# Kernel tuning notes

Measured on AMD Instinct MI355X. Metric: run time of the kernel, lower is better.

Reference implementation:

```python
import jax, jax.numpy as jnp
import numpy as np


def _mlp2(x, W1, b1, W2, b2):
    # ReluMLP with two Dense layers: relu between layers, linear output
    return jax.nn.relu(x @ W1 + b1) @ W2 + b2


def setup_inputs() -> dict:
    key = jax.random.key(0)
    N, NP, DIN, D = 100000, 25000, 16, 64
    E, EDS, EP, EUS = 1_600_000, 800_000, 400_000, 200_000
    L = 8  # number of message-passing layers actually used
    ks = iter(jax.random.split(key, 40))
    nrm = lambda shape: jax.random.normal(next(ks), shape, jnp.float32) * 0.05
    ri = lambda n, hi: jax.random.randint(next(ks), (n,), 0, hi)
    return dict(
        x=jax.random.normal(next(ks), (N, DIN), jnp.float32),
        We1=nrm((DIN, D)), be1=jnp.zeros((D,), jnp.float32),
        We2=nrm((D, D)), be2=jnp.zeros((D,), jnp.float32),
        Wm1=nrm((L, D, D)), bm1=jnp.zeros((L, D), jnp.float32),
        Wm2=nrm((L, D, D)), bm2=jnp.zeros((L, D), jnp.float32),
        Wn1=nrm((L, 2 * D, D)), bn1=jnp.zeros((L, D), jnp.float32),
        Wn2=nrm((L, D, D)), bn2=jnp.zeros((L, D), jnp.float32),
        Wd1=nrm((D, D)), bd1=jnp.zeros((D,), jnp.float32),
        Wd2=nrm((D, 2)), bd2=jnp.zeros((2,), jnp.float32),
        s_fine=ri(E, N), r_fine=ri(E, N),
        s_ds=ri(EDS, N), r_ds=ri(EDS, N),
        s_p=ri(EP, NP), r_p=ri(EP, NP),
        s_us=ri(EUS, NP), r_us=ri(EUS, NP),
        uppool=ri(N, NP), downpool=ri(NP, NP),
    )


def reference(x, We1, be1, We2, be2, Wm1, bm1, Wm2, bm2, Wn1, bn1, Wn2, bn2,
              Wd1, bd1, Wd2, bd2, s_fine, r_fine, s_ds, r_ds, s_p, r_p,
              s_us, r_us, uppool, downpool):
    def mp(l, h, s, r, n):
        # LinearMessagePassingLayer: message MLP on sender feats,
        # sum-scatter to receivers (mean_aggr=False), node MLP on [h, aggr]
        msg = _mlp2(h[s], Wm1[l], bm1[l], Wm2[l], bm2[l])          # [E, D]
        aggr = jax.ops.segment_sum(msg, r, num_segments=n)          # [n, D]
        return _mlp2(jnp.concatenate([h, aggr], -1),
                     Wn1[l], bn1[l], Wn2[l], bn2[l])                # [n, D]

    N = x.shape[0]
    NP = downpool.shape[0]
    # encode
    h = _mlp2(x, We1, be1, We2, be2)                                 # [N, D]
    h = mp(0, h, s_fine, r_fine, N)
    h = mp(1, h, s_fine, r_fine, N)
    skip = h
    # Downsample: gather by uppool idx, MP on downsampling graph, select pooled
    g = mp(2, h[uppool], s_ds, r_ds, N)                              # [N, D]
    hp = g[downpool]                                                 # [NP, D]
    # bottleneck
    hp = mp(3, hp, s_p, r_p, NP)
    hp = mp(4, hp, s_p, r_p, NP)
    # Upsample: gather by downpool idx, MP on upsampling graph, select by uppool
    g = mp(5, hp[downpool], s_us, r_us, NP)                          # [NP, D]
    h = g[uppool]                                                    # [N, D]
    # decode with skip connections
    h = mp(6, h, s_fine, r_fine, N) + skip
    h = mp(7, h, s_fine, r_fine, N) + skip
    return _mlp2(h, Wd1, bd1, Wd2, bd2)                              # [N, 2]
```

## Files before the change

### kernel.cpp

```cpp
#include <hip/hip_runtime.h>

#define WG 256

#define MLP_FMA16(ACC, A, W) do { \
    ACC[0][0]=fmaf(A.x,W.x,ACC[0][0]); ACC[0][1]=fmaf(A.x,W.y,ACC[0][1]); \
    ACC[0][2]=fmaf(A.x,W.z,ACC[0][2]); ACC[0][3]=fmaf(A.x,W.w,ACC[0][3]); \
    ACC[1][0]=fmaf(A.y,W.x,ACC[1][0]); ACC[1][1]=fmaf(A.y,W.y,ACC[1][1]); \
    ACC[1][2]=fmaf(A.y,W.z,ACC[1][2]); ACC[1][3]=fmaf(A.y,W.w,ACC[1][3]); \
    ACC[2][0]=fmaf(A.z,W.x,ACC[2][0]); ACC[2][1]=fmaf(A.z,W.y,ACC[2][1]); \
    ACC[2][2]=fmaf(A.z,W.z,ACC[2][2]); ACC[2][3]=fmaf(A.z,W.w,ACC[2][3]); \
    ACC[3][0]=fmaf(A.w,W.x,ACC[3][0]); ACC[3][1]=fmaf(A.w,W.y,ACC[3][1]); \
    ACC[3][2]=fmaf(A.w,W.z,ACC[3][2]); ACC[3][3]=fmaf(A.w,W.w,ACC[3][3]); \
} while (0)

template<int DINA, bool HAS_B, bool HAS_SKIP, bool GATHER_A,
         int MSG_DOUT, bool PARTIAL_MSG, bool WRITE_OUT1>
__global__ __launch_bounds__(WG)
void mlp2_fused(const float* __restrict__ inA, const int* __restrict__ gidxA,
                const float* __restrict__ inB,
                const float* __restrict__ W1, const float* __restrict__ b1,
                const float* __restrict__ W2, const float* __restrict__ b2,
                const float* __restrict__ skip, float* __restrict__ out1,
                const float* __restrict__ M1, const float* __restrict__ mb1,
                const float* __restrict__ M2, const float* __restrict__ mb2,
                float* __restrict__ outM, int msgN, int n)
{
    constexpr int XP = 68;
    __shared__ __align__(16) float sXT[64][XP];
    __shared__ __align__(16) float sW[64 * 64];
    __shared__ float sb[128];
    __shared__ float sW2d[128];
    __shared__ float sb2d[2];

    const int tid = threadIdx.x;
    const int tx = tid & 15, ty = tid >> 4;
    const int c0 = tx * 4, r0 = ty * 4;
    const int row0 = blockIdx.x * 64;
    const int lrow = tid & 63;
    const int kq0 = (tid >> 6) * 4;

    for (int i = tid * 4; i < DINA * 64; i += WG * 4)
        *(float4*)&sW[i] = *(const float4*)&W1[i];
    if (tid < 64) sb[tid] = b1[tid];
    else if (tid < 128) sb[tid] = b2[tid - 64];

    {
        const int rg = min(row0 + lrow, n - 1);
        const int ra = GATHER_A ? gidxA[rg] : rg;
        const float* pA = inA + (size_t)ra * DINA;
        #pragma unroll
        for (int kq = kq0; kq < DINA; kq += 16) {
            const float4 v = *(const float4*)(pA + kq);
            sXT[kq + 0][lrow] = v.x; sXT[kq + 1][lrow] = v.y;
            sXT[kq + 2][lrow] = v.z; sXT[kq + 3][lrow] = v.w;
        }
    }
    __syncthreads();

    float acc[4][4] = {};
    #pragma unroll 8
    for (int k = 0; k < DINA; ++k) {
        const float4 a = *(const float4*)&sXT[k][r0];
        const float4 w = *(const float4*)&sW[k * 64 + c0];
        MLP_FMA16(acc, a, w);
    }

    if constexpr (HAS_B) {
        __syncthreads();
        for (int i = tid * 4; i < 64 * 64; i += WG * 4)
            *(float4*)&sW[i] = *(const float4*)&W1[DINA * 64 + i];
        {
            const int rg = min(row0 + lrow, n - 1);
            const float* pB = inB + (size_t)rg * 64;
            #pragma unroll
            for (int kq = kq0; kq < 64; kq += 16) {
                const float4 v = *(const float4*)(pB + kq);
                sXT[kq + 0][lrow] = v.x; sXT[kq + 1][lrow] = v.y;
                sXT[kq + 2][lrow] = v.z; sXT[kq + 3][lrow] = v.w;
            }
        }
        __syncthreads();
        #pragma unroll 8
        for (int k = 0; k < 64; ++k) {
            const float4 a = *(const float4*)&sXT[k][r0];
            const float4 w = *(const float4*)&sW[k * 64 + c0];
            MLP_FMA16(acc, a, w);
        }
    }
    __syncthreads();

    for (int i = tid * 4; i < 64 * 64; i += WG * 4)
        *(float4*)&sW[i] = *(const float4*)&W2[i];
    #pragma unroll
    for (int j = 0; j < 4; ++j) {
        const float bj = sb[c0 + j];
        *(float4*)&sXT[c0 + j][r0] = make_float4(
            fmaxf(acc[0][j] + bj, 0.f), fmaxf(acc[1][j] + bj, 0.f),
            fmaxf(acc[2][j] + bj, 0.f), fmaxf(acc[3][j] + bj, 0.f));
    }
    __syncthreads();

    float acc2[4][4] = {};
    #pragma unroll 8
    for (int k = 0; k < 64; ++k) {
        const float4 a = *(const float4*)&sXT[k][r0];
        const float4 w = *(const float4*)&sW[k * 64 + c0];
        MLP_FMA16(acc2, a, w);
    }

    float ofull[4][4];
    #pragma unroll
    for (int i = 0; i < 4; ++i) {
        const int row = row0 + r0 + i;
        float4 s = make_float4(0.f, 0.f, 0.f, 0.f);
        if (HAS_SKIP && row < n) s = *(const float4*)&skip[(size_t)row * 64 + c0];
        ofull[i][0] = acc2[i][0] + sb[64 + c0 + 0] + s.x;
        ofull[i][1] = acc2[i][1] + sb[64 + c0 + 1] + s.y;
        ofull[i][2] = acc2[i][2] + sb[64 + c0 + 2] + s.z;
        ofull[i][3] = acc2[i][3] + sb[64 + c0 + 3] + s.w;
        if (WRITE_OUT1 && row < n)
            *(float4*)&out1[(size_t)row * 64 + c0] =
                make_float4(ofull[i][0], ofull[i][1], ofull[i][2], ofull[i][3]);
    }

    if constexpr (MSG_DOUT > 0) {
        if (!PARTIAL_MSG || row0 < msgN) {
            __syncthreads();
            for (int i = tid * 4; i < 64 * 64; i += WG * 4)
                *(float4*)&sW[i] = *(const float4*)&M1[i];
            if (tid < 64) sb[tid] = mb1[tid];
            if constexpr (MSG_DOUT == 64) {
                if (tid >= 64 && tid < 128) sb[tid] = mb2[tid - 64];
            } else {
                if (tid >= 64 && tid < 192) sW2d[tid - 64] = M2[tid - 64];
                if (tid >= 192 && tid < 194) sb2d[tid - 192] = mb2[tid - 192];
            }
            #pragma unroll
            for (int j = 0; j < 4; ++j)
                *(float4*)&sXT[c0 + j][r0] =
                    make_float4(ofull[0][j], ofull[1][j], ofull[2][j], ofull[3][j]);
            __syncthreads();

            float acc3[4][4] = {};
            #pragma unroll 8
            for (int k = 0; k < 64; ++k) {
                const float4 a = *(const float4*)&sXT[k][r0];
                const float4 w = *(const float4*)&sW[k * 64 + c0];
                MLP_FMA16(acc3, a, w);
            }
            __syncthreads();
            if constexpr (MSG_DOUT == 64) {
                for (int i = tid * 4; i < 64 * 64; i += WG * 4)
                    *(float4*)&sW[i] = *(const float4*)&M2[i];
            }
            #pragma unroll
            for (int j = 0; j < 4; ++j) {
                const float bj = sb[c0 + j];
                *(float4*)&sXT[c0 + j][r0] = make_float4(
                    fmaxf(acc3[0][j] + bj, 0.f), fmaxf(acc3[1][j] + bj, 0.f),
                    fmaxf(acc3[2][j] + bj, 0.f), fmaxf(acc3[3][j] + bj, 0.f));
            }
            __syncthreads();

            if constexpr (MSG_DOUT == 64) {
                float accM[4][4] = {};
                #pragma unroll 8
                for (int k = 0; k < 64; ++k) {
                    const float4 a = *(const float4*)&sXT[k][r0];
                    const float4 w = *(const float4*)&sW[k * 64 + c0];
                    MLP_FMA16(accM, a, w);
                }
                #pragma unroll
                for (int i = 0; i < 4; ++i) {
                    const int row = row0 + r0 + i;
                    if (row < msgN)
                        *(float4*)&outM[(size_t)row * 64 + c0] =
                            make_float4(accM[i][0] + sb[64 + c0 + 0],
                                        accM[i][1] + sb[64 + c0 + 1],
                                        accM[i][2] + sb[64 + c0 + 2],
                                        accM[i][3] + sb[64 + c0 + 3]);
                }
            } else {
                if (tid < 128) {
                    const int lr = tid >> 1, col = tid & 1;
                    float o0 = sb2d[col], o1 = 0.0f;
                    #pragma unroll 8
                    for (int k = 0; k < 64; k += 2) {
                        o0 = fmaf(sXT[k][lr],     sW2d[k * 2 + col],       o0);
                        o1 = fmaf(sXT[k + 1][lr], sW2d[(k + 1) * 2 + col], o1);
                    }
                    const int row = row0 + lr;
                    if (row < msgN) outM[(size_t)row * 2 + col] = o0 + o1;
                }
            }
        }
    }
}

template<int DINA, bool HAS_B, bool HAS_SKIP, bool GATHER_A>
__global__ __launch_bounds__(WG)
void mlp2_rt(const float* __restrict__ inA, const int* __restrict__ gidxA,
             const float* __restrict__ inB,
             const float* __restrict__ W1, const float* __restrict__ b1,
             const float* __restrict__ W2, const float* __restrict__ b2,
             const float* __restrict__ skip,
             float* __restrict__ out, int n)
{
    constexpr int XP = 68;
    __shared__ __align__(16) float sXT[64][XP];
    __shared__ __align__(16) float sW[64 * 64];
    __shared__ float sb[128];

    const int tid = threadIdx.x;
    const int tx = tid & 15, ty = tid >> 4;
    const int c0 = tx * 4, r0 = ty * 4;
    const int row0 = blockIdx.x * 64;
    const int lrow = tid & 63;
    const int kq0 = (tid >> 6) * 4;

    for (int i = tid * 4; i < DINA * 64; i += WG * 4)
        *(float4*)&sW[i] = *(const float4*)&W1[i];
    if (tid < 64) sb[tid] = b1[tid];
    else if (tid < 128) sb[tid] = b2[tid - 64];

    {
        const int rg = min(row0 + lrow, n - 1);
        const int ra = GATHER_A ? gidxA[rg] : rg;
        const float* pA = inA + (size_t)ra * DINA;
        #pragma unroll
        for (int kq = kq0; kq < DINA; kq += 16) {
            const float4 v = *(const float4*)(pA + kq);
            sXT[kq + 0][lrow] = v.x; sXT[kq + 1][lrow] = v.y;
            sXT[kq + 2][lrow] = v.z; sXT[kq + 3][lrow] = v.w;
        }
    }
    __syncthreads();

    float acc[4][4] = {};
    #pragma unroll 8
    for (int k = 0; k < DINA; ++k) {
        const float4 a = *(const float4*)&sXT[k][r0];
        const float4 w = *(const float4*)&sW[k * 64 + c0];
        MLP_FMA16(acc, a, w);
    }
    if constexpr (HAS_B) {
        __syncthreads();
        for (int i = tid * 4; i < 64 * 64; i += WG * 4)
            *(float4*)&sW[i] = *(const float4*)&W1[DINA * 64 + i];
        {
            const int rg = min(row0 + lrow, n - 1);
            const float* pB = inB + (size_t)rg * 64;
            #pragma unroll
            for (int kq = kq0; kq < 64; kq += 16) {
                const float4 v = *(const float4*)(pB + kq);
                sXT[kq + 0][lrow] = v.x; sXT[kq + 1][lrow] = v.y;
                sXT[kq + 2][lrow] = v.z; sXT[kq + 3][lrow] = v.w;
            }
        }
        __syncthreads();
        #pragma unroll 8
        for (int k = 0; k < 64; ++k) {
            const float4 a = *(const float4*)&sXT[k][r0];
            const float4 w = *(const float4*)&sW[k * 64 + c0];
            MLP_FMA16(acc, a, w);
        }
    }
    __syncthreads();

    for (int i = tid * 4; i < 64 * 64; i += WG * 4)
        *(float4*)&sW[i] = *(const float4*)&W2[i];
    #pragma unroll
    for (int j = 0; j < 4; ++j) {
        const float bj = sb[c0 + j];
        *(float4*)&sXT[c0 + j][r0] = make_float4(
            fmaxf(acc[0][j] + bj, 0.f), fmaxf(acc[1][j] + bj, 0.f),
            fmaxf(acc[2][j] + bj, 0.f), fmaxf(acc[3][j] + bj, 0.f));
    }
    __syncthreads();

    float acc2[4][4] = {};
    #pragma unroll 8
    for (int k = 0; k < 64; ++k) {
        const float4 a = *(const float4*)&sXT[k][r0];
        const float4 w = *(const float4*)&sW[k * 64 + c0];
        MLP_FMA16(acc2, a, w);
    }
    #pragma unroll
    for (int i = 0; i < 4; ++i) {
        const int row = row0 + r0 + i;
        if (row < n) {
            float4 o = make_float4(acc2[i][0] + sb[64 + c0 + 0],
                                   acc2[i][1] + sb[64 + c0 + 1],
                                   acc2[i][2] + sb[64 + c0 + 2],
                                   acc2[i][3] + sb[64 + c0 + 3]);
            if (HAS_SKIP) {
                const float4 s = *(const float4*)&skip[(size_t)row * 64 + c0];
                o.x += s.x; o.y += s.y; o.z += s.z; o.w += s.w;
            }
            *(float4*)&out[(size_t)row * 64 + c0] = o;
        }
    }
}

__global__ __launch_bounds__(WG)
void slot_fill_xcd_k(const int* __restrict__ s, const int* __restrict__ r,
                     int* __restrict__ cursor, int* __restrict__ slots,
                     int cap, int E, int n)
{
    const int xcd = blockIdx.x & 7;
    const int w   = blockIdx.x >> 3;
    const int W   = gridDim.x >> 3;
    const int lo  = (int)(((long)n * xcd) >> 3);
    const int hi  = (int)(((long)n * (xcd + 1)) >> 3);
    const int chunk = (E + W - 1) / W;
    const int e0 = w * chunk;
    const int e1 = min(E, e0 + chunk);
    for (int e = e0 + (int)threadIdx.x; e < e1; e += WG) {
        const int v = __builtin_nontemporal_load(&r[e]);
        if (v >= lo && v < hi) {
            const int sv = __builtin_nontemporal_load(&s[e]);
            const int p = atomicAdd(&cursor[v], 1);
            if (p < cap) slots[(size_t)v * cap + p] = sv;
        }
    }
}

template<bool REMAP>
__global__ __launch_bounds__(WG)
void gather_slots_k(const int* __restrict__ deg, const int* __restrict__ slots,
                    int cap, const int* __restrict__ remap,
                    const float* __restrict__ tab, float* __restrict__ aggr, int n)
{
    const int node = blockIdx.x * (WG / 64) + (threadIdx.x >> 6);
    const int c = threadIdx.x & 63;
    if (node >= n) return;
    const int d = min(deg[node], cap);
    const int* sl = slots + (size_t)node * cap;

    int myidx = 0;
    if (c < d) {
        myidx = __builtin_nontemporal_load(&sl[c]);
        if (REMAP) myidx = remap[myidx];
    }

    float a[8] = {};
    int j = 0;
    for (; j + 7 < d; j += 8) {
        #pragma unroll
        for (int u = 0; u < 8; ++u) {
            const int t = __shfl(myidx, j + u);
            a[u] += tab[(size_t)t * 64 + c];
        }
    }
    #pragma unroll 4
    for (; j < d; ++j) {
        const int t = __shfl(myidx, j);
        a[j & 7] += tab[(size_t)t * 64 + c];
    }
    aggr[(size_t)node * 64 + c] =
        ((a[0] + a[1]) + (a[2] + a[3])) + ((a[4] + a[5]) + (a[6] + a[7]));
}

extern "C" void kernel_launch(void* const* d_in, const int* in_sizes, int n_in,
                              void* d_out, int out_size, void* d_ws, size_t ws_size,
                              hipStream_t stream)
{
    const float* x    = (const float*)d_in[0];
    const float* We1  = (const float*)d_in[1];
    const float* be1  = (const float*)d_in[2];
    const float* We2  = (const float*)d_in[3];
    const float* be2  = (const float*)d_in[4];
    const float* Wm1  = (const float*)d_in[5];
    const float* bm1  = (const float*)d_in[6];
    const float* Wm2  = (const float*)d_in[7];
    const float* bm2  = (const float*)d_in[8];
    const float* Wn1  = (const float*)d_in[9];
    const float* bn1  = (const float*)d_in[10];
    const float* Wn2  = (const float*)d_in[11];
    const float* bn2  = (const float*)d_in[12];
    const float* Wd1  = (const float*)d_in[13];
    const float* bd1  = (const float*)d_in[14];
    const float* Wd2  = (const float*)d_in[15];
    const float* bd2  = (const float*)d_in[16];
    const int* s_fine = (const int*)d_in[17];
    const int* r_fine = (const int*)d_in[18];
    const int* s_ds   = (const int*)d_in[19];
    const int* r_ds   = (const int*)d_in[20];
    const int* s_p    = (const int*)d_in[21];
    const int* r_p    = (const int*)d_in[22];
    const int* s_us   = (const int*)d_in[23];
    const int* r_us   = (const int*)d_in[24];
    const int* uppool   = (const int*)d_in[25];
    const int* downpool = (const int*)d_in[26];

    const int N   = in_sizes[0] / 16;
    const int E   = in_sizes[17];
    const int EDS = in_sizes[19];
    const int EP  = in_sizes[21];
    const int EUS = in_sizes[23];
    const int NP  = in_sizes[26];

    const int CAP_FINE = 48, CAP_DS = 32, CAP_PP = 48, CAP_US = 32;

    float* B0  = (float*)d_ws;
    float* B1  = B0 + (size_t)N * 64;
    float* B2  = B1 + (size_t)N * 64;
    float* B3  = B2 + (size_t)N * 64;
    float* HPa = B3 + (size_t)N * 64;
    float* HPb = HPa + (size_t)NP * 64;
    int* ip = (int*)(HPb + (size_t)NP * 64);
    auto alloc_i = [&](size_t n) { int* p = ip; ip += n; return p; };
    int* cur_fine = alloc_i(N);
    int* cur_ds   = alloc_i(N);
    int* cur_pp   = alloc_i(NP);
    int* cur_us   = alloc_i(NP);
    int* sl_fine  = alloc_i((size_t)N * CAP_FINE);
    int* sl_ds    = alloc_i((size_t)N * CAP_DS);
    int* sl_pp    = alloc_i((size_t)NP * CAP_PP);
    int* sl_us    = alloc_i((size_t)NP * CAP_US);

    const int gN  = (N + 63) / 64;
    const int gNP = (NP + 63) / 64;
    const int gaN  = (N + 3) / 4;
    const int gaNP = (NP + 3) / 4;

    hipMemsetAsync(cur_fine, 0, (size_t)(2 * N + 2 * NP) * sizeof(int), stream);
    slot_fill_xcd_k<<<2048, WG, 0, stream>>>(s_fine, r_fine, cur_fine, sl_fine, CAP_FINE, E,   N);
    slot_fill_xcd_k<<<1024, WG, 0, stream>>>(s_ds,   r_ds,   cur_ds,   sl_ds,   CAP_DS,   EDS, N);
    slot_fill_xcd_k<<<512,  WG, 0, stream>>>(s_p,    r_p,    cur_pp,   sl_pp,   CAP_PP,   EP,  NP);
    slot_fill_xcd_k<<<512,  WG, 0, stream>>>(s_us,   r_us,   cur_us,   sl_us,   CAP_US,   EUS, NP);

    mlp2_fused<16,false,false,false,64,false,true><<<gN,WG,0,stream>>>(
        x,nullptr,nullptr, We1,be1,We2,be2, nullptr,B0,
        Wm1+0*4096,bm1+0*64,Wm2+0*4096,bm2+0*64, B1, N, N);
    gather_slots_k<false><<<gaN,WG,0,stream>>>(cur_fine,sl_fine,CAP_FINE,nullptr,B1,B2,N);

    mlp2_fused<64,true,false,false,64,false,true><<<gN,WG,0,stream>>>(
        B0,nullptr,B2, Wn1+0*8192,bn1+0*64,Wn2+0*4096,bn2+0*64, nullptr,B3,
        Wm1+1*4096,bm1+1*64,Wm2+1*4096,bm2+1*64, B0, N, N);
    gather_slots_k<false><<<gaN,WG,0,stream>>>(cur_fine,sl_fine,CAP_FINE,nullptr,B0,B2,N);

    mlp2_fused<64,true,false,false,64,true,true><<<gN,WG,0,stream>>>(
        B3,nullptr,B2, Wn1+1*8192,bn1+1*64,Wn2+1*4096,bn2+1*64, nullptr,B1,
        Wm1+2*4096,bm1+2*64,Wm2+2*4096,bm2+2*64, B0, NP, N);
    gather_slots_k<true><<<gaN,WG,0,stream>>>(cur_ds,sl_ds,CAP_DS,uppool,B0,B2,N);

    mlp2_rt<64,true,false,true><<<gN,WG,0,stream>>>(
        B1,uppool,B2, Wn1+2*8192,bn1+2*64,Wn2+2*4096,bn2+2*64, nullptr,B3,N);

    mlp2_rt<64,false,false,true><<<gNP,WG,0,stream>>>(
        B3,downpool,nullptr, Wm1+3*4096,bm1+3*64,Wm2+3*4096,bm2+3*64, nullptr,HPa,NP);
    gather_slots_k<false><<<gaNP,WG,0,stream>>>(cur_pp,sl_pp,CAP_PP,nullptr,HPa,B2,NP);

    mlp2_fused<64,true,false,true,64,false,true><<<gNP,WG,0,stream>>>(
        B3,downpool,B2, Wn1+3*8192,bn1+3*64,Wn2+3*4096,bn2+3*64, nullptr,HPb,
        Wm1+4*4096,bm1+4*64,Wm2+4*4096,bm2+4*64, HPa, NP, NP);
    gather_slots_k<false><<<gaNP,WG,0,stream>>>(cur_pp,sl_pp,CAP_PP,nullptr,HPa,B2,NP);

    mlp2_fused<64,true,false,false,64,false,true><<<gNP,WG,0,stream>>>(
        HPb,nullptr,B2, Wn1+4*8192,bn1+4*64,Wn2+4*4096,bn2+4*64, nullptr,HPa,
        Wm1+5*4096,bm1+5*64,Wm2+5*4096,bm2+5*64, HPb, NP, NP);
    gather_slots_k<true><<<gaNP,WG,0,stream>>>(cur_us,sl_us,CAP_US,downpool,HPb,B2,NP);

    mlp2_fused<64,true,false,true,64,false,true><<<gNP,WG,0,stream>>>(
        HPa,downpool,B2, Wn1+5*8192,bn1+5*64,Wn2+5*4096,bn2+5*64, nullptr,HPb,
        Wm1+6*4096,bm1+6*64,Wm2+6*4096,bm2+6*64, B3, NP, NP);
    gather_slots_k<true><<<gaN,WG,0,stream>>>(cur_fine,sl_fine,CAP_FINE,uppool,B3,B2,N);

    mlp2_fused<64,true,true,true,64,false,true><<<gN,WG,0,stream>>>(
        HPb,uppool,B2, Wn1+6*8192,bn1+6*64,Wn2+6*4096,bn2+6*64, B1,B0,
        Wm1+7*4096,bm1+7*64,Wm2+7*4096,bm2+7*64, B3, N, N);
    gather_slots_k<false><<<gaN,WG,0,stream>>>(cur_fine,sl_fine,CAP_FINE,nullptr,B3,B2,N);

    mlp2_fused<64,true,true,false,2,false,false><<<gN,WG,0,stream>>>(
        B0,nullptr,B2, Wn1+7*8192,bn1+7*64,Wn2+7*4096,bn2+7*64, B1,nullptr,
        Wd1,bd1,Wd2,bd2, (float*)d_out, N, N);
}
```

Before: 1.064 ms.

## Fuse slot-based neighbor aggregation into node-MLP kernels, drop separate gather kernels

```diff
diff --git a/kernel.cpp b/kernel.cpp
--- a/kernel.cpp
+++ b/kernel.cpp
@@ -13,11 +13,13 @@
     ACC[3][2]=fmaf(A.w,W.z,ACC[3][2]); ACC[3][3]=fmaf(A.w,W.w,ACC[3][3]); \
 } while (0)
 
-template<int DINA, bool HAS_B, bool HAS_SKIP, bool GATHER_A,
+template<int DINA, bool HAS_AGGR, bool REMAPB, bool HAS_SKIP, bool GATHER_A,
          int MSG_DOUT, bool PARTIAL_MSG, bool WRITE_OUT1>
 __global__ __launch_bounds__(WG)
 void mlp2_fused(const float* __restrict__ inA, const int* __restrict__ gidxA,
-                const float* __restrict__ inB,
+                const int* __restrict__ deg, const int* __restrict__ slots,
+                int cap, const int* __restrict__ remapB,
+                const float* __restrict__ tab,
                 const float* __restrict__ W1, const float* __restrict__ b1,
                 const float* __restrict__ W2, const float* __restrict__ b2,
                 const float* __restrict__ skip, float* __restrict__ out1,
@@ -36,8 +38,9 @@
     const int tx = tid & 15, ty = tid >> 4;
     const int c0 = tx * 4, r0 = ty * 4;
     const int row0 = blockIdx.x * 64;
-    const int lrow = tid & 63;
-    const int kq0 = (tid >> 6) * 4;
+    const int lane = tid & 63;
+    const int wv = tid >> 6;
+    const int kq0 = wv * 4;
 
     for (int i = tid * 4; i < DINA * 64; i += WG * 4)
         *(float4*)&sW[i] = *(const float4*)&W1[i];
@@ -45,14 +48,46 @@
     else if (tid < 128) sb[tid] = b2[tid - 64];
 
     {
-        const int rg = min(row0 + lrow, n - 1);
+        const int rg = min(row0 + lane, n - 1);
         const int ra = GATHER_A ? gidxA[rg] : rg;
         const float* pA = inA + (size_t)ra * DINA;
         #pragma unroll
         for (int kq = kq0; kq < DINA; kq += 16) {
             const float4 v = *(const float4*)(pA + kq);
-            sXT[kq + 0][lrow] = v.x; sXT[kq + 1][lrow] = v.y;
-            sXT[kq + 2][lrow] = v.z; sXT[kq + 3][lrow] = v.w;
+            sXT[kq + 0][lane] = v.x; sXT[kq + 1][lane] = v.y;
+            sXT[kq + 2][lane] = v.z; sXT[kq + 3][lane] = v.w;
+        }
+    }
+
+    float av[16];
+    if constexpr (HAS_AGGR) {
+        #pragma unroll
+        for (int i = 0; i < 16; ++i) {
+            const int node = min(row0 + wv * 16 + i, n - 1);
+            const int d = min(deg[node], cap);
+            const int* sl = slots + (size_t)node * cap;
+            int myidx = 0;
+            if (lane < d) {
+                myidx = sl[lane];
+                if (REMAPB) myidx = remapB[myidx];
+            }
+            float a0 = 0.f, a1 = 0.f, a2 = 0.f, a3 = 0.f;
+            int j = 0;
+            for (; j + 3 < d; j += 4) {
+                const int t0 = __shfl(myidx, j + 0);
+                const int t1 = __shfl(myidx, j + 1);
+                const int t2 = __shfl(myidx, j + 2);
+                const int t3 = __shfl(myidx, j + 3);
+                a0 += tab[(size_t)t0 * 64 + lane];
+                a1 += tab[(size_t)t1 * 64 + lane];
+                a2 += tab[(size_t)t2 * 64 + lane];
+                a3 += tab[(size_t)t3 * 64 + lane];
+            }
+            for (; j < d; ++j) {
+                const int t = __shfl(myidx, j);
+                a0 += tab[(size_t)t * 64 + lane];
+            }
+            av[i] = (a0 + a1) + (a2 + a3);
         }
     }
     __syncthreads();
@@ -65,20 +100,13 @@
         MLP_FMA16(acc, a, w);
     }
 
-    if constexpr (HAS_B) {
+    if constexpr (HAS_AGGR) {
         __syncthreads();
         for (int i = tid * 4; i < 64 * 64; i += WG * 4)
             *(float4*)&sW[i] = *(const float4*)&W1[DINA * 64 + i];
-        {
-            const int rg = min(row0 + lrow, n - 1);
-            const float* pB = inB + (size_t)rg * 64;
-            #pragma unroll
-            for (int kq = kq0; kq < 64; kq += 16) {
-                const float4 v = *(const float4*)(pB + kq);
-                sXT[kq + 0][lrow] = v.x; sXT[kq + 1][lrow] = v.y;
-                sXT[kq + 2][lrow] = v.z; sXT[kq + 3][lrow] = v.w;
-            }
-        }
+        #pragma unroll
+        for (int i = 0; i < 16; ++i)
+            sXT[lane][wv * 16 + i] = av[i];
         __syncthreads();
         #pragma unroll 8
         for (int k = 0; k < 64; ++k) {
@@ -128,12 +156,13 @@
             __syncthreads();
             for (int i = tid * 4; i < 64 * 64; i += WG * 4)
                 *(float4*)&sW[i] = *(const float4*)&M1[i];
-            if (tid < 64) sb[tid] = mb1[tid];
             if constexpr (MSG_DOUT == 64) {
-                if (tid >= 64 && tid < 128) sb[tid] = mb2[tid - 64];
+                if (tid < 64) sb[tid] = mb1[tid];
+                else if (tid < 128) sb[tid] = mb2[tid - 64];
             } else {
-                if (tid >= 64 && tid < 192) sW2d[tid - 64] = M2[tid - 64];
-                if (tid >= 192 && tid < 194) sb2d[tid - 192] = mb2[tid - 192];
+                if (tid < 64) sb[tid] = mb1[tid];
+                else if (tid < 192) sW2d[tid - 64] = M2[tid - 64];
+                else if (tid < 194) sb2d[tid - 192] = mb2[tid - 192];
             }
             #pragma unroll
             for (int j = 0; j < 4; ++j)
@@ -197,111 +226,6 @@
     }
 }
 
-template<int DINA, bool HAS_B, bool HAS_SKIP, bool GATHER_A>
-__global__ __launch_bounds__(WG)
-void mlp2_rt(const float* __restrict__ inA, const int* __restrict__ gidxA,
-             const float* __restrict__ inB,
-             const float* __restrict__ W1, const float* __restrict__ b1,
-             const float* __restrict__ W2, const float* __restrict__ b2,
-             const float* __restrict__ skip,
-             float* __restrict__ out, int n)
-{
-    constexpr int XP = 68;
-    __shared__ __align__(16) float sXT[64][XP];
-    __shared__ __align__(16) float sW[64 * 64];
-    __shared__ float sb[128];
-
-    const int tid = threadIdx.x;
-    const int tx = tid & 15, ty = tid >> 4;
-    const int c0 = tx * 4, r0 = ty * 4;
-    const int row0 = blockIdx.x * 64;
-    const int lrow = tid & 63;
-    const int kq0 = (tid >> 6) * 4;
-
-    for (int i = tid * 4; i < DINA * 64; i += WG * 4)
-        *(float4*)&sW[i] = *(const float4*)&W1[i];
-    if (tid < 64) sb[tid] = b1[tid];
-    else if (tid < 128) sb[tid] = b2[tid - 64];
-
-    {
-        const int rg = min(row0 + lrow, n - 1);
-        const int ra = GATHER_A ? gidxA[rg] : rg;
-        const float* pA = inA + (size_t)ra * DINA;
-        #pragma unroll
-        for (int kq = kq0; kq < DINA; kq += 16) {
-            const float4 v = *(const float4*)(pA + kq);
-            sXT[kq + 0][lrow] = v.x; sXT[kq + 1][lrow] = v.y;
-            sXT[kq + 2][lrow] = v.z; sXT[kq + 3][lrow] = v.w;
-        }
-    }
-    __syncthreads();
-
-    float acc[4][4] = {};
-    #pragma unroll 8
-    for (int k = 0; k < DINA; ++k) {
-        const float4 a = *(const float4*)&sXT[k][r0];
-        const float4 w = *(const float4*)&sW[k * 64 + c0];
-        MLP_FMA16(acc, a, w);
-    }
-    if constexpr (HAS_B) {
-        __syncthreads();
-        for (int i = tid * 4; i < 64 * 64; i += WG * 4)
-            *(float4*)&sW[i] = *(const float4*)&W1[DINA * 64 + i];
-        {
-            const int rg = min(row0 + lrow, n - 1);
-            const float* pB = inB + (size_t)rg * 64;
-            #pragma unroll
-            for (int kq = kq0; kq < 64; kq += 16) {
-                const float4 v = *(const float4*)(pB + kq);
-                sXT[kq + 0][lrow] = v.x; sXT[kq + 1][lrow] = v.y;
-                sXT[kq + 2][lrow] = v.z; sXT[kq + 3][lrow] = v.w;
-            }
-        }
-        __syncthreads();
-        #pragma unroll 8
-        for (int k = 0; k < 64; ++k) {
-            const float4 a = *(const float4*)&sXT[k][r0];
-            const float4 w = *(const float4*)&sW[k * 64 + c0];
-            MLP_FMA16(acc, a, w);
-        }
-    }
-    __syncthreads();
-
-    for (int i = tid * 4; i < 64 * 64; i += WG * 4)
-        *(float4*)&sW[i] = *(const float4*)&W2[i];
-    #pragma unroll
-    for (int j = 0; j < 4; ++j) {
-        const float bj = sb[c0 + j];
-        *(float4*)&sXT[c0 + j][r0] = make_float4(
-            fmaxf(acc[0][j] + bj, 0.f), fmaxf(acc[1][j] + bj, 0.f),
-            fmaxf(acc[2][j] + bj, 0.f), fmaxf(acc[3][j] + bj, 0.f));
-    }
-    __syncthreads();
-
-    float acc2[4][4] = {};
-    #pragma unroll 8
-    for (int k = 0; k < 64; ++k) {
-        const float4 a = *(const float4*)&sXT[k][r0];
-        const float4 w = *(const float4*)&sW[k * 64 + c0];
-        MLP_FMA16(acc2, a, w);
-    }
-    #pragma unroll
-    for (int i = 0; i < 4; ++i) {
-        const int row = row0 + r0 + i;
-        if (row < n) {
-            float4 o = make_float4(acc2[i][0] + sb[64 + c0 + 0],
-                                   acc2[i][1] + sb[64 + c0 + 1],
-                                   acc2[i][2] + sb[64 + c0 + 2],
-                                   acc2[i][3] + sb[64 + c0 + 3]);
-            if (HAS_SKIP) {
-                const float4 s = *(const float4*)&skip[(size_t)row * 64 + c0];
-                o.x += s.x; o.y += s.y; o.z += s.z; o.w += s.w;
-            }
-            *(float4*)&out[(size_t)row * 64 + c0] = o;
-        }
-    }
-}
-
 __global__ __launch_bounds__(WG)
 void slot_fill_xcd_k(const int* __restrict__ s, const int* __restrict__ r,
                      int* __restrict__ cursor, int* __restrict__ slots,
@@ -323,42 +247,6 @@
             if (p < cap) slots[(size_t)v * cap + p] = sv;
         }
     }
-}
-
-template<bool REMAP>
-__global__ __launch_bounds__(WG)
-void gather_slots_k(const int* __restrict__ deg, const int* __restrict__ slots,
-                    int cap, const int* __restrict__ remap,
-                    const float* __restrict__ tab, float* __restrict__ aggr, int n)
-{
-    const int node = blockIdx.x * (WG / 64) + (threadIdx.x >> 6);
-    const int c = threadIdx.x & 63;
-    if (node >= n) return;
-    const int d = min(deg[node], cap);
-    const int* sl = slots + (size_t)node * cap;
-
-    int myidx = 0;
-    if (c < d) {
-        myidx = __builtin_nontemporal_load(&sl[c]);
-        if (REMAP) myidx = remap[myidx];
-    }
-
-    float a[8] = {};
-    int j = 0;
-    for (; j + 7 < d; j += 8) {
-        #pragma unroll
-        for (int u = 0; u < 8; ++u) {
-            const int t = __shfl(myidx, j + u);
-            a[u] += tab[(size_t)t * 64 + c];
-        }
-    }
-    #pragma unroll 4
-    for (; j < d; ++j) {
-        const int t = __shfl(myidx, j);
-        a[j & 7] += tab[(size_t)t * 64 + c];
-    }
-    aggr[(size_t)node * 64 + c] =
-        ((a[0] + a[1]) + (a[2] + a[3])) + ((a[4] + a[5]) + (a[6] + a[7]));
 }
 
 extern "C" void kernel_launch(void* const* d_in, const int* in_sizes, int n_in,
@@ -421,8 +309,6 @@
 
     const int gN  = (N + 63) / 64;
     const int gNP = (NP + 63) / 64;
-    const int gaN  = (N + 3) / 4;
-    const int gaNP = (NP + 3) / 4;
 
     hipMemsetAsync(cur_fine, 0, (size_t)(2 * N + 2 * NP) * sizeof(int), stream);
     slot_fill_xcd_k<<<2048, WG, 0, stream>>>(s_fine, r_fine, cur_fine, sl_fine, CAP_FINE, E,   N);
@@ -430,49 +316,59 @@
     slot_fill_xcd_k<<<512,  WG, 0, stream>>>(s_p,    r_p,    cur_pp,   sl_pp,   CAP_PP,   EP,  NP);
     slot_fill_xcd_k<<<512,  WG, 0, stream>>>(s_us,   r_us,   cur_us,   sl_us,   CAP_US,   EUS, NP);
 
-    mlp2_fused<16,false,false,false,64,false,true><<<gN,WG,0,stream>>>(
-        x,nullptr,nullptr, We1,be1,We2,be2, nullptr,B0,
+
+    mlp2_fused<16,false,false,false,false,64,false,true><<<gN,WG,0,stream>>>(
+        x,nullptr, nullptr,nullptr,0,nullptr, nullptr,
+        We1,be1,We2,be2, nullptr,B0,
         Wm1+0*4096,bm1+0*64,Wm2+0*4096,bm2+0*64, B1, N, N);
-    gather_slots_k<false><<<gaN,WG,0,stream>>>(cur_fine,sl_fine,CAP_FINE,nullptr,B1,B2,N);
-
-    mlp2_fused<64,true,false,false,64,false,true><<<gN,WG,0,stream>>>(
-        B0,nullptr,B2, Wn1+0*8192,bn1+0*64,Wn2+0*4096,bn2+0*64, nullptr,B3,
+
+    mlp2_fused<64,true,false,false,false,64,false,true><<<gN,WG,0,stream>>>(
+        B0,nullptr, cur_fine,sl_fine,CAP_FINE,nullptr, B1,
+        Wn1+0*8192,bn1+0*64,Wn2+0*4096,bn2+0*64, nullptr,B2,
         Wm1+1*4096,bm1+1*64,Wm2+1*4096,bm2+1*64, B0, N, N);
-    gather_slots_k<false><<<gaN,WG,0,stream>>>(cur_fine,sl_fine,CAP_FINE,nullptr,B0,B2,N);
-
-    mlp2_fused<64,true,false,false,64,true,true><<<gN,WG,0,stream>>>(
-        B3,nullptr,B2, Wn1+1*8192,bn1+1*64,Wn2+1*4096,bn2+1*64, nullptr,B1,
-        Wm1+2*4096,bm1+2*64,Wm2+2*4096,bm2+2*64, B0, NP, N);
-    gather_slots_k<true><<<gaN,WG,0,stream>>>(cur_ds,sl_ds,CAP_DS,uppool,B0,B2,N);
-
-    mlp2_rt<64,true,false,true><<<gN,WG,0,stream>>>(
-        B1,uppool,B2, Wn1+2*8192,bn1+2*64,Wn2+2*4096,bn2+2*64, nullptr,B3,N);
-
-    mlp2_rt<64,false,false,true><<<gNP,WG,0,stream>>>(
-        B3,downpool,nullptr, Wm1+3*4096,bm1+3*64,Wm2+3*4096,bm2+3*64, nullptr,HPa,NP);
-    gather_slots_k<false><<<gaNP,WG,0,stream>>>(cur_pp,sl_pp,CAP_PP,nullptr,HPa,B2,NP);
-
-    mlp2_fused<64,true,false,true,64,false,true><<<gNP,WG,0,stream>>>(
-        B3,downpool,B2, Wn1+3*8192,bn1+3*64,Wn2+3*4096,bn2+3*64, nullptr,HPb,
-        Wm1+4*4096,bm1+4*64,Wm2+4*4096,bm2+4*64, HPa, NP, NP);
-    gather_slots_k<false><<<gaNP,WG,0,stream>>>(cur_pp,sl_pp,CAP_PP,nullptr,HPa,B2,NP);
-
-    mlp2_fused<64,true,false,false,64,false,true><<<gNP,WG,0,stream>>>(
-        HPb,nullptr,B2, Wn1+4*8192,bn1+4*64,Wn2+4*4096,bn2+4*64, nullptr,HPa,
+
+    mlp2_fused<64,true,false,false,false,64,true,true><<<gN,WG,0,stream>>>(
+        B2,nullptr, cur_fine,sl_fine,CAP_FINE,nullptr, B0,
+        Wn1+1*8192,bn1+1*64,Wn2+1*4096,bn2+1*64, nullptr,B1,
+        Wm1+2*4096,bm1+2*64,Wm2+2*4096,bm2+2*64, B2, NP, N);
+
+    mlp2_fused<64,true,true,false,true,0,false,true><<<gN,WG,0,stream>>>(
+        B1,uppool, cur_ds,sl_ds,CAP_DS,uppool, B2,
+        Wn1+2*8192,bn1+2*64,Wn2+2*4096,bn2+2*64, nullptr,B3,
+        nullptr,nullptr,nullptr,nullptr, nullptr, 0, N);
+
+    mlp2_fused<64,false,false,false,true,0,false,true><<<gNP,WG,0,stream>>>(
+        B3,downpool, nullptr,nullptr,0,nullptr, nullptr,
+        Wm1+3*4096,bm1+3*64,Wm2+3*4096,bm2+3*64, nullptr,HPa,
+        nullptr,nullptr,nullptr,nullptr, nullptr, 0, NP);
+
+    mlp2_fused<64,true,false,false,true,64,false,true><<<gNP,WG,0,stream>>>(
+        B3,downpool, cur_pp,sl_pp,CAP_PP,nullptr, HPa,
+        Wn1+3*8192,bn1+3*64,Wn2+3*4096,bn2+3*64, nullptr,HPb,
+        Wm1+4*4096,bm1+4*64,Wm2+4*4096,bm2+4*64, B2, NP, NP);
+
+    mlp2_fused<64,true,false,false,false,64,false,true><<<gNP,WG,0,stream>>>(
+        HPb,nullptr, cur_pp,sl_pp,CAP_PP,nullptr, B2,
+        Wn1+4*8192,bn1+4*64,Wn2+4*4096,bn2+4*64, nullptr,HPa,
         Wm1+5*4096,bm1+5*64,Wm2+5*4096,bm2+5*64, HPb, NP, NP);
-    gather_slots_k<true><<<gaNP,WG,0,stream>>>(cur_us,sl_us,CAP_US,downpool,HPb,B2,NP);
-
-    mlp2_fused<64,true,false,true,64,false,true><<<gNP,WG,0,stream>>>(
-        HPa,downpool,B2, Wn1+5*8192,bn1+5*64,Wn2+5*4096,bn2+5*64, nullptr,HPb,
-        Wm1+6*4096,bm1+6*64,Wm2+6*4096,bm2+6*64, B3, NP, NP);
-    gather_slots_k<true><<<gaN,WG,0,stream>>>(cur_fine,sl_fine,CAP_FINE,uppool,B3,B2,N);
-
-    mlp2_fused<64,true,true,true,64,false,true><<<gN,WG,0,stream>>>(
-        HPb,uppool,B2, Wn1+6*8192,bn1+6*64,Wn2+6*4096,bn2+6*64, B1,B0,
-        Wm1+7*4096,bm1+7*64,Wm2+7*4096,bm2+7*64, B3, N, N);
-    gather_slots_k<false><<<gaN,WG,0,stream>>>(cur_fine,sl_fine,CAP_FINE,nullptr,B3,B2,N);
-
-    mlp2_fused<64,true,true,false,2,false,false><<<gN,WG,0,stream>>>(
-        B0,nullptr,B2, Wn1+7*8192,bn1+7*64,Wn2+7*4096,bn2+7*64, B1,nullptr,
+
+    mlp2_fused<64,true,true,false,true,64,false,true><<<gNP,WG,0,stream>>>(
+        HPa,downpool, cur_us,sl_us,CAP_US,downpool, HPb,
+        Wn1+5*8192,bn1+5*64,Wn2+5*4096,bn2+5*64, nullptr,B3,
+        Wm1+6*4096,bm1+6*64,Wm2+6*4096,bm2+6*64, B2, NP, NP);
+
+    mlp2_fused<64,true,true,true,true,0,false,true><<<gN,WG,0,stream>>>(
+        B3,uppool, cur_fine,sl_fine,CAP_FINE,uppool, B2,
+        Wn1+6*8192,bn1+6*64,Wn2+6*4096,bn2+6*64, B1,B0,
+        nullptr,nullptr,nullptr,nullptr, nullptr, 0, N);
+
+    mlp2_fused<64,false,false,false,false,0,false,true><<<gN,WG,0,stream>>>(
+        B0,nullptr, nullptr,nullptr,0,nullptr, nullptr,
+        Wm1+7*4096,bm1+7*64,Wm2+7*4096,bm2+7*64, nullptr,B3,
+        nullptr,nullptr,nullptr,nullptr, nullptr, 0, N);
+
+    mlp2_fused<64,true,false,true,false,2,false,false><<<gN,WG,0,stream>>>(
+        B0,nullptr, cur_fine,sl_fine,CAP_FINE,nullptr, B3,
+        Wn1+7*8192,bn1+7*64,Wn2+7*4096,bn2+7*64, B1,nullptr,
         Wd1,bd1,Wd2,bd2, (float*)d_out, N, N);
 }
```

New measurement: 1.235 ms. +16.1%, slower.

## Read MLP weights directly from global memory and merge slot-fill launches

Applied to the files above, without the earlier changes.

```diff
diff --git a/kernel.cpp b/kernel.cpp
--- a/kernel.cpp
+++ b/kernel.cpp
@@ -27,7 +27,6 @@
 {
     constexpr int XP = 68;
     __shared__ __align__(16) float sXT[64][XP];
-    __shared__ __align__(16) float sW[64 * 64];
     __shared__ float sb[128];
     __shared__ float sW2d[128];
     __shared__ float sb2d[2];
@@ -39,8 +38,6 @@
     const int lrow = tid & 63;
     const int kq0 = (tid >> 6) * 4;
 
-    for (int i = tid * 4; i < DINA * 64; i += WG * 4)
-        *(float4*)&sW[i] = *(const float4*)&W1[i];
     if (tid < 64) sb[tid] = b1[tid];
     else if (tid < 128) sb[tid] = b2[tid - 64];
 
@@ -61,14 +58,12 @@
     #pragma unroll 8
     for (int k = 0; k < DINA; ++k) {
         const float4 a = *(const float4*)&sXT[k][r0];
-        const float4 w = *(const float4*)&sW[k * 64 + c0];
+        const float4 w = *(const float4*)&W1[k * 64 + c0];
         MLP_FMA16(acc, a, w);
     }
 
     if constexpr (HAS_B) {
         __syncthreads();
-        for (int i = tid * 4; i < 64 * 64; i += WG * 4)
-            *(float4*)&sW[i] = *(const float4*)&W1[DINA * 64 + i];
         {
             const int rg = min(row0 + lrow, n - 1);
             const float* pB = inB + (size_t)rg * 64;
@@ -83,14 +78,12 @@
         #pragma unroll 8
         for (int k = 0; k < 64; ++k) {
             const float4 a = *(const float4*)&sXT[k][r0];
-            const float4 w = *(const float4*)&sW[k * 64 + c0];
+            const float4 w = *(const float4*)&W1[(DINA + k) * 64 + c0];
             MLP_FMA16(acc, a, w);
         }
     }
     __syncthreads();
 
-    for (int i = tid * 4; i < 64 * 64; i += WG * 4)
-        *(float4*)&sW[i] = *(const float4*)&W2[i];
     #pragma unroll
     for (int j = 0; j < 4; ++j) {
         const float bj = sb[c0 + j];
@@ -104,7 +97,7 @@
     #pragma unroll 8
     for (int k = 0; k < 64; ++k) {
         const float4 a = *(const float4*)&sXT[k][r0];
-        const float4 w = *(const float4*)&sW[k * 64 + c0];
+        const float4 w = *(const float4*)&W2[k * 64 + c0];
         MLP_FMA16(acc2, a, w);
     }
 
@@ -126,14 +119,13 @@
     if constexpr (MSG_DOUT > 0) {
         if (!PARTIAL_MSG || row0 < msgN) {
             __syncthreads();
-            for (int i = tid * 4; i < 64 * 64; i += WG * 4)
-                *(float4*)&sW[i] = *(const float4*)&M1[i];
-            if (tid < 64) sb[tid] = mb1[tid];
             if constexpr (MSG_DOUT == 64) {
-                if (tid >= 64 && tid < 128) sb[tid] = mb2[tid - 64];
+                if (tid < 64) sb[tid] = mb1[tid];
+                else if (tid < 128) sb[tid] = mb2[tid - 64];
             } else {
-                if (tid >= 64 && tid < 192) sW2d[tid - 64] = M2[tid - 64];
-                if (tid >= 192 && tid < 194) sb2d[tid - 192] = mb2[tid - 192];
+                if (tid < 64) sb[tid] = mb1[tid];
+                else if (tid < 192) sW2d[tid - 64] = M2[tid - 64];
+                else if (tid < 194) sb2d[tid - 192] = mb2[tid - 192];
             }
             #pragma unroll
             for (int j = 0; j < 4; ++j)
@@ -145,14 +137,10 @@
             #pragma unroll 8
             for (int k = 0; k < 64; ++k) {
                 const float4 a = *(const float4*)&sXT[k][r0];
-                const float4 w = *(const float4*)&sW[k * 64 + c0];
+                const float4 w = *(const float4*)&M1[k * 64 + c0];
                 MLP_FMA16(acc3, a, w);
             }
             __syncthreads();
-            if constexpr (MSG_DOUT == 64) {
-                for (int i = tid * 4; i < 64 * 64; i += WG * 4)
-                    *(float4*)&sW[i] = *(const float4*)&M2[i];
-            }
             #pragma unroll
             for (int j = 0; j < 4; ++j) {
                 const float bj = sb[c0 + j];
@@ -167,7 +155,7 @@
                 #pragma unroll 8
                 for (int k = 0; k < 64; ++k) {
                     const float4 a = *(const float4*)&sXT[k][r0];
-                    const float4 w = *(const float4*)&sW[k * 64 + c0];
+                    const float4 w = *(const float4*)&M2[k * 64 + c0];
                     MLP_FMA16(accM, a, w);
                 }
                 #pragma unroll
@@ -208,7 +196,6 @@
 {
     constexpr int XP = 68;
     __shared__ __align__(16) float sXT[64][XP];
-    __shared__ __align__(16) float sW[64 * 64];
     __shared__ float sb[128];
 
     const int tid = threadIdx.x;
@@ -218,8 +205,6 @@
     const int lrow = tid & 63;
     const int kq0 = (tid >> 6) * 4;
 
-    for (int i = tid * 4; i < DINA * 64; i += WG * 4)
-        *(float4*)&sW[i] = *(const float4*)&W1[i];
     if (tid < 64) sb[tid] = b1[tid];
     else if (tid < 128) sb[tid] = b2[tid - 64];
 
@@ -240,13 +225,11 @@
     #pragma unroll 8
     for (int k = 0; k < DINA; ++k) {
         const float4 a = *(const float4*)&sXT[k][r0];
-        const float4 w = *(const float4*)&sW[k * 64 + c0];
+        const float4 w = *(const float4*)&W1[k * 64 + c0];
         MLP_FMA16(acc, a, w);
     }
     if constexpr (HAS_B) {
         __syncthreads();
-        for (int i = tid * 4; i < 64 * 64; i += WG * 4)
-            *(float4*)&sW[i] = *(const float4*)&W1[DINA * 64 + i];
         {
             const int rg = min(row0 + lrow, n - 1);
             const float* pB = inB + (size_t)rg * 64;
@@ -261,14 +244,12 @@
         #pragma unroll 8
         for (int k = 0; k < 64; ++k) {
             const float4 a = *(const float4*)&sXT[k][r0];
-            const float4 w = *(const float4*)&sW[k * 64 + c0];
+            const float4 w = *(const float4*)&W1[(DINA + k) * 64 + c0];
             MLP_FMA16(acc, a, w);
         }
     }
     __syncthreads();
 
-    for (int i = tid * 4; i < 64 * 64; i += WG * 4)
-        *(float4*)&sW[i] = *(const float4*)&W2[i];
     #pragma unroll
     for (int j = 0; j < 4; ++j) {
         const float bj = sb[c0 + j];
@@ -282,7 +263,7 @@
     #pragma unroll 8
     for (int k = 0; k < 64; ++k) {
         const float4 a = *(const float4*)&sXT[k][r0];
-        const float4 w = *(const float4*)&sW[k * 64 + c0];
+        const float4 w = *(const float4*)&W2[k * 64 + c0];
         MLP_FMA16(acc2, a, w);
     }
     #pragma unroll
@@ -303,15 +284,21 @@
 }
 
 __global__ __launch_bounds__(WG)
-void slot_fill_xcd_k(const int* __restrict__ s, const int* __restrict__ r,
-                     int* __restrict__ cursor, int* __restrict__ slots,
-                     int cap, int E, int n)
+void slot_fill4_xcd_k(const int* __restrict__ s0, const int* __restrict__ r0, int* cu0, int* sl0, int cap0, int E0, int n0,
+                      const int* __restrict__ s1, const int* __restrict__ r1, int* cu1, int* sl1, int cap1, int E1, int n1,
+                      const int* __restrict__ s2, const int* __restrict__ r2, int* cu2, int* sl2, int cap2, int E2, int n2,
+                      const int* __restrict__ s3, const int* __restrict__ r3, int* cu3, int* sl3, int cap3, int E3, int n3,
+                      int W0, int W1n, int W2n, int W3n)
 {
     const int xcd = blockIdx.x & 7;
-    const int w   = blockIdx.x >> 3;
-    const int W   = gridDim.x >> 3;
-    const int lo  = (int)(((long)n * xcd) >> 3);
-    const int hi  = (int)(((long)n * (xcd + 1)) >> 3);
+    int w = blockIdx.x >> 3;
+    const int* s; const int* r; int* cur; int* sl; int cap; int E; int n; int W;
+    if (w < W0)              { s=s0; r=r0; cur=cu0; sl=sl0; cap=cap0; E=E0; n=n0; W=W0; }
+    else if ((w -= W0) < W1n) { s=s1; r=r1; cur=cu1; sl=sl1; cap=cap1; E=E1; n=n1; W=W1n; }
+    else if ((w -= W1n) < W2n){ s=s2; r=r2; cur=cu2; sl=sl2; cap=cap2; E=E2; n=n2; W=W2n; }
+    else { w -= W2n;           s=s3; r=r3; cur=cu3; sl=sl3; cap=cap3; E=E3; n=n3; W=W3n; }
+    const int lo = (int)(((long)n * xcd) >> 3);
+    const int hi = (int)(((long)n * (xcd + 1)) >> 3);
     const int chunk = (E + W - 1) / W;
     const int e0 = w * chunk;
     const int e1 = min(E, e0 + chunk);
@@ -319,8 +306,8 @@
         const int v = __builtin_nontemporal_load(&r[e]);
         if (v >= lo && v < hi) {
             const int sv = __builtin_nontemporal_load(&s[e]);
-            const int p = atomicAdd(&cursor[v], 1);
-            if (p < cap) slots[(size_t)v * cap + p] = sv;
+            const int p = atomicAdd(&cur[v], 1);
+            if (p < cap) sl[(size_t)v * cap + p] = sv;
         }
     }
 }
@@ -425,10 +412,15 @@
     const int gaNP = (NP + 3) / 4;
 
     hipMemsetAsync(cur_fine, 0, (size_t)(2 * N + 2 * NP) * sizeof(int), stream);
-    slot_fill_xcd_k<<<2048, WG, 0, stream>>>(s_fine, r_fine, cur_fine, sl_fine, CAP_FINE, E,   N);
-    slot_fill_xcd_k<<<1024, WG, 0, stream>>>(s_ds,   r_ds,   cur_ds,   sl_ds,   CAP_DS,   EDS, N);
-    slot_fill_xcd_k<<<512,  WG, 0, stream>>>(s_p,    r_p,    cur_pp,   sl_pp,   CAP_PP,   EP,  NP);
-    slot_fill_xcd_k<<<512,  WG, 0, stream>>>(s_us,   r_us,   cur_us,   sl_us,   CAP_US,   EUS, NP);
+    {
+        const int W0 = 256, W1n = 128, W2n = 64, W3n = 64;
+        slot_fill4_xcd_k<<<8 * (W0 + W1n + W2n + W3n), WG, 0, stream>>>(
+            s_fine, r_fine, cur_fine, sl_fine, CAP_FINE, E,   N,
+            s_ds,   r_ds,   cur_ds,   sl_ds,   CAP_DS,   EDS, N,
+            s_p,    r_p,    cur_pp,   sl_pp,   CAP_PP,   EP,  NP,
+            s_us,   r_us,   cur_us,   sl_us,   CAP_US,   EUS, NP,
+            W0, W1n, W2n, W3n);
+    }
 
     mlp2_fused<16,false,false,false,64,false,true><<<gN,WG,0,stream>>>(
         x,nullptr,nullptr, We1,be1,We2,be2, nullptr,B0,
```

After: 1.101 ms. 1.04x slower.

## Fuse four slot-fill launches with encoder and first message MLP into one kernel

Applied to the files above, without the earlier changes.

```diff
diff --git a/kernel.cpp b/kernel.cpp
--- a/kernel.cpp
+++ b/kernel.cpp
@@ -128,12 +128,13 @@
             __syncthreads();
             for (int i = tid * 4; i < 64 * 64; i += WG * 4)
                 *(float4*)&sW[i] = *(const float4*)&M1[i];
-            if (tid < 64) sb[tid] = mb1[tid];
             if constexpr (MSG_DOUT == 64) {
-                if (tid >= 64 && tid < 128) sb[tid] = mb2[tid - 64];
+                if (tid < 64) sb[tid] = mb1[tid];
+                else if (tid < 128) sb[tid] = mb2[tid - 64];
             } else {
-                if (tid >= 64 && tid < 192) sW2d[tid - 64] = M2[tid - 64];
-                if (tid >= 192 && tid < 194) sb2d[tid - 192] = mb2[tid - 192];
+                if (tid < 64) sb[tid] = mb1[tid];
+                else if (tid < 192) sW2d[tid - 64] = M2[tid - 64];
+                else if (tid < 194) sb2d[tid - 192] = mb2[tid - 192];
             }
             #pragma unroll
             for (int j = 0; j < 4; ++j)
@@ -303,25 +304,146 @@
 }
 
 __global__ __launch_bounds__(WG)
-void slot_fill_xcd_k(const int* __restrict__ s, const int* __restrict__ r,
-                     int* __restrict__ cursor, int* __restrict__ slots,
-                     int cap, int E, int n)
+void fill4_enc_k(const int* __restrict__ s0, const int* __restrict__ r0v, int* cu0, int* sl0, int cap0, int E0, int n0,
+                 const int* __restrict__ s1, const int* __restrict__ r1, int* cu1, int* sl1, int cap1, int E1, int n1,
+                 const int* __restrict__ s2, const int* __restrict__ r2, int* cu2, int* sl2, int cap2, int E2, int n2,
+                 const int* __restrict__ s3, const int* __restrict__ r3, int* cu3, int* sl3, int cap3, int E3, int n3,
+                 int W0, int W1n, int W2n, int W3n, int FILLB,
+                 const float* __restrict__ x,
+                 const float* __restrict__ We1, const float* __restrict__ be1,
+                 const float* __restrict__ We2, const float* __restrict__ be2,
+                 float* __restrict__ h0,
+                 const float* __restrict__ M1, const float* __restrict__ mb1,
+                 const float* __restrict__ M2, const float* __restrict__ mb2,
+                 float* __restrict__ msg0, int N)
 {
-    const int xcd = blockIdx.x & 7;
-    const int w   = blockIdx.x >> 3;
-    const int W   = gridDim.x >> 3;
-    const int lo  = (int)(((long)n * xcd) >> 3);
-    const int hi  = (int)(((long)n * (xcd + 1)) >> 3);
-    const int chunk = (E + W - 1) / W;
-    const int e0 = w * chunk;
-    const int e1 = min(E, e0 + chunk);
-    for (int e = e0 + (int)threadIdx.x; e < e1; e += WG) {
-        const int v = __builtin_nontemporal_load(&r[e]);
-        if (v >= lo && v < hi) {
-            const int sv = __builtin_nontemporal_load(&s[e]);
-            const int p = atomicAdd(&cursor[v], 1);
-            if (p < cap) slots[(size_t)v * cap + p] = sv;
-        }
+    constexpr int XP = 68;
+    __shared__ __align__(16) float sXT[64][XP];
+    __shared__ float sb[128];
+
+    if ((int)blockIdx.x < FILLB) {
+        const int xcd = blockIdx.x & 7;
+        int w = blockIdx.x >> 3;
+        const int* s; const int* r; int* cur; int* sl; int cap; int E; int n; int W;
+        if (w < W0)               { s=s0; r=r0v; cur=cu0; sl=sl0; cap=cap0; E=E0; n=n0; W=W0; }
+        else if ((w -= W0) < W1n) { s=s1; r=r1;  cur=cu1; sl=sl1; cap=cap1; E=E1; n=n1; W=W1n; }
+        else if ((w -= W1n) < W2n){ s=s2; r=r2;  cur=cu2; sl=sl2; cap=cap2; E=E2; n=n2; W=W2n; }
+        else { w -= W2n;            s=s3; r=r3;  cur=cu3; sl=sl3; cap=cap3; E=E3; n=n3; W=W3n; }
+        const int lo = (int)(((long)n * xcd) >> 3);
+        const int hi = (int)(((long)n * (xcd + 1)) >> 3);
+        const int chunk = (E + W - 1) / W;
+        const int e0 = w * chunk;
+        const int e1 = min(E, e0 + chunk);
+        for (int e = e0 + (int)threadIdx.x; e < e1; e += WG) {
+            const int v = __builtin_nontemporal_load(&r[e]);
+            if (v >= lo && v < hi) {
+                const int sv = __builtin_nontemporal_load(&s[e]);
+                const int p = atomicAdd(&cur[v], 1);
+                if (p < cap) sl[(size_t)v * cap + p] = sv;
+            }
+        }
+        return;
+    }
+
+    const int bid = blockIdx.x - FILLB;
+    const int tid = threadIdx.x;
+    const int tx = tid & 15, ty = tid >> 4;
+    const int c0 = tx * 4, r0 = ty * 4;
+    const int row0 = bid * 64;
+    const int lrow = tid & 63;
+    const int kq0 = (tid >> 6) * 4;
+
+    if (tid < 64) sb[tid] = be1[tid];
+    else if (tid < 128) sb[tid] = be2[tid - 64];
+
+    {
+        const int rg = min(row0 + lrow, N - 1);
+        const float* pA = x + (size_t)rg * 16;
+        const float4 v = *(const float4*)(pA + kq0);
+        sXT[kq0 + 0][lrow] = v.x; sXT[kq0 + 1][lrow] = v.y;
+        sXT[kq0 + 2][lrow] = v.z; sXT[kq0 + 3][lrow] = v.w;
+    }
+    __syncthreads();
+
+    float acc[4][4] = {};
+    #pragma unroll
+    for (int k = 0; k < 16; ++k) {
+        const float4 a = *(const float4*)&sXT[k][r0];
+        const float4 w = *(const float4*)&We1[k * 64 + c0];
+        MLP_FMA16(acc, a, w);
+    }
+    __syncthreads();
+    #pragma unroll
+    for (int j = 0; j < 4; ++j) {
+        const float bj = sb[c0 + j];
+        *(float4*)&sXT[c0 + j][r0] = make_float4(
+            fmaxf(acc[0][j] + bj, 0.f), fmaxf(acc[1][j] + bj, 0.f),
+            fmaxf(acc[2][j] + bj, 0.f), fmaxf(acc[3][j] + bj, 0.f));
+    }
+    __syncthreads();
+
+    float acc2[4][4] = {};
+    #pragma unroll 8
+    for (int k = 0; k < 64; ++k) {
+        const float4 a = *(const float4*)&sXT[k][r0];
+        const float4 w = *(const float4*)&We2[k * 64 + c0];
+        MLP_FMA16(acc2, a, w);
+    }
+    float ofull[4][4];
+    #pragma unroll
+    for (int i = 0; i < 4; ++i) {
+        const int row = row0 + r0 + i;
+        ofull[i][0] = acc2[i][0] + sb[64 + c0 + 0];
+        ofull[i][1] = acc2[i][1] + sb[64 + c0 + 1];
+        ofull[i][2] = acc2[i][2] + sb[64 + c0 + 2];
+        ofull[i][3] = acc2[i][3] + sb[64 + c0 + 3];
+        if (row < N)
+            *(float4*)&h0[(size_t)row * 64 + c0] =
+                make_float4(ofull[i][0], ofull[i][1], ofull[i][2], ofull[i][3]);
+    }
+
+    __syncthreads();
+    if (tid < 64) sb[tid] = mb1[tid];
+    else if (tid < 128) sb[tid] = mb2[tid - 64];
+    #pragma unroll
+    for (int j = 0; j < 4; ++j)
+        *(float4*)&sXT[c0 + j][r0] =
+            make_float4(ofull[0][j], ofull[1][j], ofull[2][j], ofull[3][j]);
+    __syncthreads();
+
+    float acc3[4][4] = {};
+    #pragma unroll 8
+    for (int k = 0; k < 64; ++k) {
+        const float4 a = *(const float4*)&sXT[k][r0];
+        const float4 w = *(const float4*)&M1[k * 64 + c0];
+        MLP_FMA16(acc3, a, w);
+    }
+    __syncthreads();
+    #pragma unroll
+    for (int j = 0; j < 4; ++j) {
+        const float bj = sb[c0 + j];
+        *(float4*)&sXT[c0 + j][r0] = make_float4(
+            fmaxf(acc3[0][j] + bj, 0.f), fmaxf(acc3[1][j] + bj, 0.f),
+            fmaxf(acc3[2][j] + bj, 0.f), fmaxf(acc3[3][j] + bj, 0.f));
+    }
+    __syncthreads();
+
+    float accM[4][4] = {};
+    #pragma unroll 8
+    for (int k = 0; k < 64; ++k) {
+        const float4 a = *(const float4*)&sXT[k][r0];
+        const float4 w = *(const float4*)&M2[k * 64 + c0];
+        MLP_FMA16(accM, a, w);
+    }
+    #pragma unroll
+    for (int i = 0; i < 4; ++i) {
+        const int row = row0 + r0 + i;
+        if (row < N)
+            *(float4*)&msg0[(size_t)row * 64 + c0] =
+                make_float4(accM[i][0] + sb[64 + c0 + 0],
+                            accM[i][1] + sb[64 + c0 + 1],
+                            accM[i][2] + sb[64 + c0 + 2],
+                            accM[i][3] + sb[64 + c0 + 3]);
     }
 }
 
@@ -425,14 +547,18 @@
     const int gaNP = (NP + 3) / 4;
 
     hipMemsetAsync(cur_fine, 0, (size_t)(2 * N + 2 * NP) * sizeof(int), stream);
-    slot_fill_xcd_k<<<2048, WG, 0, stream>>>(s_fine, r_fine, cur_fine, sl_fine, CAP_FINE, E,   N);
-    slot_fill_xcd_k<<<1024, WG, 0, stream>>>(s_ds,   r_ds,   cur_ds,   sl_ds,   CAP_DS,   EDS, N);
-    slot_fill_xcd_k<<<512,  WG, 0, stream>>>(s_p,    r_p,    cur_pp,   sl_pp,   CAP_PP,   EP,  NP);
-    slot_fill_xcd_k<<<512,  WG, 0, stream>>>(s_us,   r_us,   cur_us,   sl_us,   CAP_US,   EUS, NP);
-
-    mlp2_fused<16,false,false,false,64,false,true><<<gN,WG,0,stream>>>(
-        x,nullptr,nullptr, We1,be1,We2,be2, nullptr,B0,
-        Wm1+0*4096,bm1+0*64,Wm2+0*4096,bm2+0*64, B1, N, N);
+    {
+        const int W0 = 256, W1n = 128, W2n = 64, W3n = 64;
+        const int FILLB = 8 * (W0 + W1n + W2n + W3n);
+        fill4_enc_k<<<FILLB + gN, WG, 0, stream>>>(
+            s_fine, r_fine, cur_fine, sl_fine, CAP_FINE, E,   N,
+            s_ds,   r_ds,   cur_ds,   sl_ds,   CAP_DS,   EDS, N,
+            s_p,    r_p,    cur_pp,   sl_pp,   CAP_PP,   EP,  NP,
+            s_us,   r_us,   cur_us,   sl_us,   CAP_US,   EUS, NP,
+            W0, W1n, W2n, W3n, FILLB,
+            x, We1, be1, We2, be2, B0,
+            Wm1 + 0*4096, bm1 + 0*64, Wm2 + 0*4096, bm2 + 0*64, B1, N);
+    }
     gather_slots_k<false><<<gaN,WG,0,stream>>>(cur_fine,sl_fine,CAP_FINE,nullptr,B1,B2,N);
 
     mlp2_fused<64,true,false,false,64,false,true><<<gN,WG,0,stream>>>(
```

Result: no change. 1.056 ms (-0.7%).
